# Kernel optimization log

Measured on AMD Instinct MI355X. Metric: run time of the kernel, lower is better.

Reference implementation:

```python
import jax, jax.numpy as jnp
import numpy as np

INF = 1000000000.0
MU = 1e-08
SAFE_THRESHOLDS = 0.05
PARTITIONS = 8
MAX_PARTITIONS = 16
VISION_RADIUS = 2.0
NS = 100          # NORMALIZED_SIZE
B = 1024
OBS_LEN = 8
TWO_PI = 2.0 * np.pi


def setup_inputs() -> dict:
    key = jax.random.key(0)
    k1, k2, k3, k4, k5, k6 = jax.random.split(key, 6)
    seg_maps = jax.random.uniform(k1, (B, NS, NS), dtype=jnp.float32)
    # seg_map_paras = [W (2), b (2), order (2)]; W must be nonzero scale.
    W = jax.random.uniform(k2, (B, 2), minval=1.0, maxval=2.0, dtype=jnp.float32)
    b = jax.random.uniform(k3, (B, 2), minval=-5.0, maxval=5.0, dtype=jnp.float32)
    order0 = jax.random.randint(k4, (B, 1), 0, 2).astype(jnp.float32)
    order = jnp.concatenate([order0, jnp.zeros((B, 1), jnp.float32)], axis=-1)
    seg_map_paras = jnp.concatenate([W, b, order], axis=-1)
    trajectories = 2.0 * jax.random.normal(k5, (B, OBS_LEN, 2), dtype=jnp.float32)
    current_pos = 5.0 * jax.random.normal(k6, (B, 1, 2), dtype=jnp.float32)
    return {"seg_maps": seg_maps, "seg_map_paras": seg_map_paras,
            "trajectories": trajectories, "current_pos": current_pos}


def reference(seg_maps, seg_map_paras, trajectories, current_pos):
    Bn = seg_maps.shape[0]
    P = PARTITIONS
    _obs = trajectories + current_pos                      # [B, obs, 2]
    _maps = seg_maps.reshape(Bn, -1)                       # [B, NS*NS]
    safe = _maps <= SAFE_THRESHOLDS                        # [B, NS*NS] bool

    moving_vector = _obs[..., -1, :] - _obs[..., 0, :]     # [B, 2]
    moving_length = jnp.linalg.norm(moving_vector, axis=-1)  # [B]

    W = seg_map_paras[..., :2][..., None, :]               # [B, 1, 2]
    b = seg_map_paras[..., 2:4][..., None, :]              # [B, 1, 2]
    order = seg_map_paras[..., 4:6]                        # [B, 2]

    ii = jnp.arange(NS, dtype=jnp.float32)
    pix = jnp.stack(jnp.meshgrid(ii, ii, indexing='ij'), axis=-1).reshape(-1, 2)  # [NS*NS, 2]

    map_pos = (pix - b) / W                                # [B, NS*NS, 2]
    # swap x/y where order flag == 1
    map_pos = jnp.where((order[:, 0] == 1)[:, None, None], map_pos[..., ::-1], map_pos)

    direction_vectors = map_pos - current_pos              # [B, NS*NS, 2]
    distances = jnp.linalg.norm(direction_vectors, axis=-1)  # [B, NS*NS]
    angles = jnp.arctan2(direction_vectors[..., 0], direction_vectors[..., 1])
    bins = (jnp.mod(angles, TWO_PI) / (TWO_PI / P)).astype(jnp.int32)
    bins = jnp.clip(bins, 0, P - 1)                        # [B, NS*NS] int32

    equ_dis = (distances + MU) / (_maps + MU)
    r = (VISION_RADIUS * moving_length)[..., None]         # [B, 1]
    valid = (~safe) & (distances <= r)
    d = jnp.where(valid, equ_dis, INF)                     # [B, NS*NS]

    # single-pass segment-min keyed by (batch, angle bin)
    seg_ids = (jnp.arange(Bn, dtype=jnp.int32)[:, None] * P + bins).reshape(-1)
    min_d = jax.ops.segment_min(d.reshape(-1), seg_ids, num_segments=Bn * P)
    min_d = jnp.minimum(min_d.reshape(Bn, P), INF)         # empty bins -> INF

    obstacle_mask = (min_d < INF).astype(jnp.float32)      # [B, P]
    f_velocity = moving_length[:, None] * obstacle_mask
    f_min_distance = min_d * obstacle_mask
    bin_centers = TWO_PI * (jnp.arange(P, dtype=jnp.float32) + 0.5) / P
    f_direction = bin_centers[None, :] * obstacle_mask

    pc = jnp.stack([f_velocity, f_min_distance, f_direction], axis=-1)  # [B, P, 3]
    pc = jnp.pad(pc, ((0, 0), (0, MAX_PARTITIONS - P), (0, 0)))
    return pc
```

## Files before the change

kernel.cpp:

```cpp
#include <hip/hip_runtime.h>


#define INFV 1.0e9f

__global__ __launch_bounds__(256)
void pcl_kernel(const float* __restrict__ seg_maps,
                const float* __restrict__ paras,
                const float* __restrict__ traj,
                const float* __restrict__ cpos,
                float* __restrict__ out)
{
    const int b    = blockIdx.x;
    const int tid  = threadIdx.x;
    const int lane = tid & 63;
    const int wave = tid >> 6;

    __shared__ __align__(16) float sRow[100];
    __shared__ __align__(16) float sCol[100];
    __shared__ __align__(16) float sCol2[100];
    __shared__ float sred[4][8];

    const float* pp = paras + b * 6;
    const float W0 = pp[0], W1 = pp[1];
    const float bb0 = pp[2], bb1 = pp[3];
    const bool  swp = (pp[4] == 1.0f);
    const float cp0 = cpos[b * 2 + 0];
    const float cp1 = cpos[b * 2 + 1];

    const float* tp  = traj + b * 16;
    const float o00 = __fadd_rn(tp[0],  cp0);
    const float o01 = __fadd_rn(tp[1],  cp1);
    const float o70 = __fadd_rn(tp[14], cp0);
    const float o71 = __fadd_rn(tp[15], cp1);
    const float mv0 = __fsub_rn(o70, o00);
    const float mv1 = __fsub_rn(o71, o01);
    const float mlen = sqrtf(__fadd_rn(__fmul_rn(mv0, mv0), __fmul_rn(mv1, mv1)));
    const float r    = __fmul_rn(2.0f, mlen);
    const float r2m  = __fmul_rn(r, r) * 1.00002f + 1e-30f;

    if (tid < 100) {
        const float a = ((float)tid - bb0) / W0;
        sRow[tid] = __fsub_rn(a, swp ? cp1 : cp0);
    } else if (tid < 200) {
        const int j = tid - 100;
        const float c = ((float)j - bb1) / W1;
        const float cv = __fsub_rn(c, swp ? cp0 : cp1);
        sCol[j]  = cv;
        sCol2[j] = __fmul_rn(cv, cv);
    }
    __syncthreads();

    float m[8];
#pragma unroll
    for (int o = 0; o < 8; ++o) m[o] = INFV;

    const float* smap = seg_maps + (size_t)b * 10000;

    for (int q = tid; q < 2500; q += 256) {
        const int k0 = q << 2;
        const int i  = k0 / 100;
        const int j0 = k0 - i * 100;

        const float4 mp = *reinterpret_cast<const float4*>(smap + k0);
        const float  rv = sRow[i];
        const float x2r = __fmul_rn(rv, rv);
        const float4 c2 = *reinterpret_cast<const float4*>(&sCol2[j0]);

        const float mapv[4] = {mp.x, mp.y, mp.z, mp.w};
        const float c2s[4]  = {c2.x, c2.y, c2.z, c2.w};
        float d2[4];
        bool  anyp = false;
#pragma unroll
        for (int c = 0; c < 4; ++c) {
            d2[c] = __fadd_rn(x2r, c2s[c]);
            anyp |= (mapv[c] > 0.05f) && (d2[c] <= r2m);
        }
        if (__any(anyp)) {
            const float4 cv4 = *reinterpret_cast<const float4*>(&sCol[j0]);
            const float cvs[4] = {cv4.x, cv4.y, cv4.z, cv4.w};
#pragma unroll
            for (int c = 0; c < 4; ++c) {
                const float colv = cvs[c];
                const float x = swp ? colv : rv;
                const float y = swp ? rv : colv;
                const float dd = sqrtf(d2[c]);
                const bool val = (mapv[c] > 0.05f) && (dd <= r);
                const int bin =
                    (y > 0.0f)
                      ? ((x >= 0.0f) ? ((x < y) ? 0 : 1)
                                     : ((-x > y) ? 6 : 7))
                      : ((y < 0.0f)
                           ? ((x > 0.0f) ? ((x > -y) ? 2 : 3)
                                         : ((x > y) ? 4 : 5))
                           : ((x > 0.0f) ? 2
                              : ((x < 0.0f) ? 6
                                 : ((__float_as_uint(y) & 0x80000000u) ? 4 : 0))));
                const float e  = __fdividef(__fadd_rn(dd, 1.0e-8f),
                                            __fadd_rn(mapv[c], 1.0e-8f));
                const float dv = val ? e : INFV;
#pragma unroll
                for (int o = 0; o < 8; ++o)
                    m[o] = fminf(m[o], (bin == o) ? dv : INFV);
            }
        }
    }

#pragma unroll
    for (int o = 0; o < 8; ++o) {
        float v = m[o];
#pragma unroll
        for (int off = 32; off > 0; off >>= 1)
            v = fminf(v, __shfl_down(v, off, 64));
        if (lane == 0) sred[wave][o] = v;
    }
    __syncthreads();

    if (tid < 16) {
        float vel = 0.0f, md = 0.0f, dir = 0.0f;
        if (tid < 8) {
            const float v = fminf(fminf(sred[0][tid], sred[1][tid]),
                                  fminf(sred[2][tid], sred[3][tid]));
            if (v < INFV) {
                vel = mlen;
                md  = v;
                dir = __fmul_rn(6.28318530717958647692f,
                                __fmul_rn((float)tid + 0.5f, 0.125f));
            }
        }
        float* po = out + (size_t)b * 48 + tid * 3;
        po[0] = vel; po[1] = md; po[2] = dir;
    }
}

extern "C" void kernel_launch(void* const* d_in, const int* in_sizes, int n_in,
                              void* d_out, int out_size, void* d_ws, size_t ws_size,
                              hipStream_t stream) {
    const float* seg_maps = (const float*)d_in[0];
    const float* paras    = (const float*)d_in[1];
    const float* traj     = (const float*)d_in[2];
    const float* cpos     = (const float*)d_in[3];
    float* out            = (float*)d_out;

    const int B = in_sizes[1] / 6;
    pcl_kernel<<<B, 256, 0, stream>>>(seg_maps, paras, traj, cpos, out);
}
```

Baseline: 86.53 us.

## Restrict scan to radius bounding box and reduce bins with LDS atomics

Computes, per batch, the row and column index ranges whose squared offset lies within the vision radius, then scans only that bounding box of the segmentation map instead of all pixels. The per-thread 8-bin register minima and wave shuffle reduction are replaced by LDS atomicMin on the float bit patterns, which is valid because the values are positive. This skips global loads and arithmetic outside the radius. In exchange, loads become scalar and possibly uncoalesced, and atomic contention and extra barriers are added.

```diff
diff --git a/kernel.cpp b/kernel.cpp
--- a/kernel.cpp
+++ b/kernel.cpp
@@ -10,15 +10,14 @@
                 const float* __restrict__ cpos,
                 float* __restrict__ out)
 {
-    const int b    = blockIdx.x;
-    const int tid  = threadIdx.x;
-    const int lane = tid & 63;
-    const int wave = tid >> 6;
+    const int b   = blockIdx.x;
+    const int tid = threadIdx.x;
 
     __shared__ __align__(16) float sRow[100];
     __shared__ __align__(16) float sCol[100];
     __shared__ __align__(16) float sCol2[100];
-    __shared__ float sred[4][8];
+    __shared__ int sILo, sIHi, sJLo, sJHi;
+    __shared__ unsigned sMin[8];
 
     const float* pp = paras + b * 6;
     const float W0 = pp[0], W1 = pp[1];
@@ -38,88 +37,75 @@
     const float r    = __fmul_rn(2.0f, mlen);
     const float r2m  = __fmul_rn(r, r) * 1.00002f + 1e-30f;
 
+    if (tid == 0) { sILo = 1000; sIHi = -1; sJLo = 1000; sJHi = -1; }
+    if (tid < 8)  sMin[tid] = __float_as_uint(INFV);
+    __syncthreads();
+
     if (tid < 100) {
-        const float a = ((float)tid - bb0) / W0;
-        sRow[tid] = __fsub_rn(a, swp ? cp1 : cp0);
+        const float a  = ((float)tid - bb0) / W0;
+        const float rv = __fsub_rn(a, swp ? cp1 : cp0);
+        sRow[tid] = rv;
+        if (__fmul_rn(rv, rv) <= r2m) {
+            atomicMin(&sILo, tid);
+            atomicMax(&sIHi, tid);
+        }
     } else if (tid < 200) {
         const int j = tid - 100;
-        const float c = ((float)j - bb1) / W1;
+        const float c  = ((float)j - bb1) / W1;
         const float cv = __fsub_rn(c, swp ? cp0 : cp1);
+        const float cv2 = __fmul_rn(cv, cv);
         sCol[j]  = cv;
-        sCol2[j] = __fmul_rn(cv, cv);
+        sCol2[j] = cv2;
+        if (cv2 <= r2m) {
+            atomicMin(&sJLo, j);
+            atomicMax(&sJHi, j);
+        }
     }
     __syncthreads();
 
-    float m[8];
-#pragma unroll
-    for (int o = 0; o < 8; ++o) m[o] = INFV;
+    const int ilo = sILo, ihi = sIHi;
+    const int jlo = sJLo, jhi = sJHi;
 
-    const float* smap = seg_maps + (size_t)b * 10000;
-
-    for (int q = tid; q < 2500; q += 256) {
-        const int k0 = q << 2;
-        const int i  = k0 / 100;
-        const int j0 = k0 - i * 100;
-
-        const float4 mp = *reinterpret_cast<const float4*>(smap + k0);
-        const float  rv = sRow[i];
-        const float x2r = __fmul_rn(rv, rv);
-        const float4 c2 = *reinterpret_cast<const float4*>(&sCol2[j0]);
-
-        const float mapv[4] = {mp.x, mp.y, mp.z, mp.w};
-        const float c2s[4]  = {c2.x, c2.y, c2.z, c2.w};
-        float d2[4];
-        bool  anyp = false;
-#pragma unroll
-        for (int c = 0; c < 4; ++c) {
-            d2[c] = __fadd_rn(x2r, c2s[c]);
-            anyp |= (mapv[c] > 0.05f) && (d2[c] <= r2m);
-        }
-        if (__any(anyp)) {
-            const float4 cv4 = *reinterpret_cast<const float4*>(&sCol[j0]);
-            const float cvs[4] = {cv4.x, cv4.y, cv4.z, cv4.w};
-#pragma unroll
-            for (int c = 0; c < 4; ++c) {
-                const float colv = cvs[c];
-                const float x = swp ? colv : rv;
-                const float y = swp ? rv : colv;
-                const float dd = sqrtf(d2[c]);
-                const bool val = (mapv[c] > 0.05f) && (dd <= r);
-                const int bin =
-                    (y > 0.0f)
-                      ? ((x >= 0.0f) ? ((x < y) ? 0 : 1)
-                                     : ((-x > y) ? 6 : 7))
-                      : ((y < 0.0f)
-                           ? ((x > 0.0f) ? ((x > -y) ? 2 : 3)
-                                         : ((x > y) ? 4 : 5))
-                           : ((x > 0.0f) ? 2
-                              : ((x < 0.0f) ? 6
-                                 : ((__float_as_uint(y) & 0x80000000u) ? 4 : 0))));
-                const float e  = __fdividef(__fadd_rn(dd, 1.0e-8f),
-                                            __fadd_rn(mapv[c], 1.0e-8f));
-                const float dv = val ? e : INFV;
-#pragma unroll
-                for (int o = 0; o < 8; ++o)
-                    m[o] = fminf(m[o], (bin == o) ? dv : INFV);
+    if (ihi >= 0 && jhi >= 0) {
+        const float* smap = seg_maps + (size_t)b * 10000;
+        const int w   = jhi - jlo + 1;
+        const int tot = (ihi - ilo + 1) * w;
+        for (int p = tid; p < tot; p += 256) {
+            const int pi = (int)((unsigned)p / (unsigned)w);
+            const int i  = ilo + pi;
+            const int j  = jlo + (p - pi * w);
+            const float mapv = smap[i * 100 + j];
+            const float rv = sRow[i];
+            const float d2 = __fadd_rn(__fmul_rn(rv, rv), sCol2[j]);
+            if ((mapv > 0.05f) && (d2 <= r2m)) {
+                const float dd = sqrtf(d2);
+                if (dd <= r) {
+                    const float colv = sCol[j];
+                    const float x = swp ? colv : rv;
+                    const float y = swp ? rv : colv;
+                    const int bin =
+                        (y > 0.0f)
+                          ? ((x >= 0.0f) ? ((x < y) ? 0 : 1)
+                                         : ((-x > y) ? 6 : 7))
+                          : ((y < 0.0f)
+                               ? ((x > 0.0f) ? ((x > -y) ? 2 : 3)
+                                             : ((x > y) ? 4 : 5))
+                               : ((x > 0.0f) ? 2
+                                  : ((x < 0.0f) ? 6
+                                     : ((__float_as_uint(y) & 0x80000000u) ? 4 : 0))));
+                    const float e = __fdividef(__fadd_rn(dd, 1.0e-8f),
+                                               __fadd_rn(mapv, 1.0e-8f));
+                    atomicMin(&sMin[bin], __float_as_uint(e));
+                }
             }
         }
-    }
-
-#pragma unroll
-    for (int o = 0; o < 8; ++o) {
-        float v = m[o];
-#pragma unroll
-        for (int off = 32; off > 0; off >>= 1)
-            v = fminf(v, __shfl_down(v, off, 64));
-        if (lane == 0) sred[wave][o] = v;
     }
     __syncthreads();
 
     if (tid < 16) {
         float vel = 0.0f, md = 0.0f, dir = 0.0f;
         if (tid < 8) {
-            const float v = fminf(fminf(sred[0][tid], sred[1][tid]),
-                                  fminf(sred[2][tid], sred[3][tid]));
+            const float v = __uint_as_float(sMin[tid]);
             if (v < INFV) {
                 vel = mlen;
                 md  = v;
```

After: 86.81 us. No clear change (+0.3%).
